# Kernel optimization log

Hardware: AMD Instinct MI355X
Metric: run time of the kernel (lower is better)

## Reference

```python
import jax, jax.numpy as jnp
import numpy as np


def _next_pow2(n: int) -> int:
    # matches torch: 2 ** ceil(log2(n))
    return 1 << (int(n) - 1).bit_length()


def setup_inputs() -> dict:
    key = jax.random.key(0)
    k1, k2 = jax.random.split(key)
    B, T, L = 256, 32768, 32768
    x = jax.random.normal(k1, (B, T), dtype=jnp.float32)
    filt = jax.random.normal(k2, (1, L), dtype=jnp.float32)
    return {"x": x, "filt": filt}


def reference(x, filt):
    """EpochedFutureFill.forward: exact causal convolution of x with filt.

    The per-token epoched algorithm (tau-step direct sum + FutureFill FFT
    cache refresh every K steps, cache initialized to zero) computes exactly
    y[b, t] = sum_{s=0}^{min(t, L-1)} filt[0, s] * x[b, t-s].
    We compute it with one FFT-based linear convolution, mirroring the
    float32 FFT math of future_fill().
    """
    B, T = x.shape
    L = filt.shape[-1]
    n_fft = _next_pow2(T + L - 1)
    xf = jnp.fft.rfft(x.astype(jnp.float32), n=n_fft)          # (B, n_fft//2+1)
    wf = jnp.fft.rfft(filt.astype(jnp.float32), n=n_fft)       # (1, n_fft//2+1)
    y = jnp.fft.irfft(xf * wf, n=n_fft)[:, :T]                 # causal lags 0..T-1
    return y.astype(x.dtype)
```

## Files before the change

### kernel.cpp

```cpp
#include <hip/hip_runtime.h>
#include <cstdint>

typedef __attribute__((ext_vector_type(8))) short short8;
typedef __attribute__((ext_vector_type(4))) float floatx4;

#define TWO_PI 6.283185307179586f

__device__ __forceinline__ unsigned short f2bf(float f) {
  union { float f; uint32_t u; } c; c.f = f;
  uint32_t u = c.u;
  u += 0x7FFFu + ((u >> 16) & 1u);
  return (unsigned short)(u >> 16);
}
__device__ __forceinline__ uint32_t packbf(float re, float im) {
  return (uint32_t)f2bf(re) | ((uint32_t)f2bf(im) << 16);
}


__global__ __launch_bounds__(256) void prep_all(
    const float* __restrict__ x, const float* __restrict__ filt,
    unsigned short* __restrict__ A1, unsigned short* __restrict__ A2,
    unsigned short* __restrict__ A3, unsigned short* __restrict__ A4,
    uint32_t* __restrict__ Zp, float2* __restrict__ Gw,
    float2* __restrict__ Tw) {
  const int bid = blockIdx.x;
  const int tid = threadIdx.x;
  const float w256 = TWO_PI / 256.0f;
  if (bid < 3072) {
    int idx = bid * 256 + tid;
    if (idx < 131072) {
      int col = idx & 255, row = idx >> 8;
      int k1 = row >> 1, d = row & 1, r = col >> 1, e = col & 1;
      float th = (float)((k1 * r) & 255) * w256;
      float sn, cs; __sincosf(th, &sn, &cs);
      A1[idx] = f2bf(d == 0 ? (e == 0 ? cs : sn) : (e == 0 ? -sn : cs));
    } else if (idx < 393216) {
      int j = idx - 131072;
      int col = j & 511, row = j >> 9;
      int k2 = row >> 1, d = row & 1, cc = col >> 1, e = col & 1;
      float th = (float)((k2 * cc) & 255) * w256;
      float sn, cs; __sincosf(th, &sn, &cs);
      A2[j] = f2bf(d == 0 ? (e == 0 ? cs : sn) : (e == 0 ? -sn : cs));
    } else if (idx < 655360) {
      int j = idx - 393216;
      int col = j & 511, row = j >> 9;
      int cc = row >> 1, d = row & 1, k2 = col >> 1, e = col & 1;
      float th = (float)((k2 * cc) & 255) * w256;
      float sn, cs; __sincosf(th, &sn, &cs);
      A3[j] = f2bf(d == 0 ? (e == 0 ? cs : -sn) : (e == 0 ? sn : cs));
    } else {
      int j = idx - 655360;
      int col = j & 511, row = j >> 9;
      int r = row >> 1, d = row & 1, k1 = col >> 1, e = col & 1;
      float th = (float)((k1 * r) & 255) * w256;
      float sn, cs; __sincosf(th, &sn, &cs);
      A4[j] = f2bf(d == 0 ? (e == 0 ? cs : -sn) : (e == 0 ? sn : cs));
    }
  } else if (bid < 4096) {
    int b2 = bid - 3072;
    int s = b2 >> 3, rq = b2 & 7;
    const float* x0 = x + (size_t)(2 * s) * 32768;
    const float* x1 = x0 + 32768;
    uint32_t v[16];
    #pragma unroll
    for (int rr = 0; rr < 16; ++rr) {
      int t = tid + 256 * (rq * 16 + rr);
      v[rr] = (uint32_t)f2bf(x0[t]) | ((uint32_t)f2bf(x1[t]) << 16);
    }
    uint32_t* dst = Zp + (size_t)(s * 256 + tid) * 128 + rq * 16;
    #pragma unroll
    for (int j = 0; j < 16; j += 4)
      *(uint4*)(dst + j) = make_uint4(v[j], v[j + 1], v[j + 2], v[j + 3]);
  } else if (bid < 4352) {
    int k1 = bid - 4096, c = tid;
    float ar = 0.f, ai = 0.f;
    for (int r = 0; r < 128; ++r) {
      float v = filt[c + 256 * r];
      float th = (float)((k1 * r) & 255) * w256;
      float sn, cs; __sincosf(th, &sn, &cs);
      ar += v * cs; ai -= v * sn;
    }
    float th = (float)((k1 * c) & 65535) * (TWO_PI / 65536.0f);
    float sn, cs; __sincosf(th, &sn, &cs);
    Gw[(k1 << 8) + c] = make_float2(ar * cs + ai * sn, ai * cs - ar * sn);
  } else {
    int k1 = bid - 4352, c = tid;
    float th = (float)((k1 * c) & 65535) * (TWO_PI / 65536.0f);
    float sn, cs; __sincosf(th, &sn, &cs);
    Tw[(k1 << 8) + c] = make_float2(cs, sn);
  }
}

__global__ __launch_bounds__(256) void prep_wb(const float2* __restrict__ Gw,
                                               float2* __restrict__ WtT) {
  int k1 = blockIdx.x, k2 = threadIdx.x;
  float ar = 0.f, ai = 0.f;
  for (int c = 0; c < 256; ++c) {
    float2 g = Gw[(k1 << 8) + c];
    float th = (float)((k2 * c) & 255) * (TWO_PI / 256.0f);
    float sn, cs; __sincosf(th, &sn, &cs);
    ar += g.x * cs + g.y * sn;
    ai += g.y * cs - g.x * sn;
  }
  WtT[(k2 << 8) + k1] = make_float2(ar, ai);
}

template <int MODE, int NCHUNK>
__global__ __launch_bounds__(256, 4) void dft_stage(
    const unsigned short* __restrict__ Af,
    const unsigned short* __restrict__ Bd,
    uint32_t* __restrict__ outp,
    float* __restrict__ yout,
    const float2* __restrict__ tab) {
  __shared__ unsigned short Sm[16384];
  constexpr int KP = NCHUNK * 32;

  const int mt = blockIdx.x >> 8;
  const int nt = blockIdx.x & 255;
  const int m0 = mt * 128, n0 = nt * 128;

  const int tid = threadIdx.x;
  const int w = tid >> 6, lane = tid & 63;
  const int qlo = lane & 15, qhi = lane >> 4;
  const int wr = w >> 1, wc = w & 1;
  const int rsub = lane >> 2;
  const int koff = ((lane & 3) ^ ((lane >> 3) & 3)) << 3;

  floatx4 acc[4][4];
  #pragma unroll
  for (int i = 0; i < 4; ++i)
    #pragma unroll
    for (int j = 0; j < 4; ++j) acc[i][j] = (floatx4){0.f, 0.f, 0.f, 0.f};

  auto issue = [&](int t) {
    const int buf = t & 1;
    const int k0 = t * 32;
    unsigned short* Asb = Sm + buf * 4096;
    unsigned short* Bsb = Sm + 8192 + buf * 4096;
    #pragma unroll
    for (int q = 0; q < 2; ++q) {
      const int rowbase = w * 32 + q * 16;
      const int R = rowbase + rsub;
      const unsigned short* gA = Af + (size_t)(m0 + R) * KP + k0 + koff;
      const unsigned short* gB = Bd + (size_t)(n0 + R) * KP + k0 + koff;
      __builtin_amdgcn_global_load_lds(
          (const __attribute__((address_space(1))) uint32_t*)gA,
          (__attribute__((address_space(3))) uint32_t*)&Asb[rowbase * 32], 16, 0, 0);
      __builtin_amdgcn_global_load_lds(
          (const __attribute__((address_space(1))) uint32_t*)gB,
          (__attribute__((address_space(3))) uint32_t*)&Bsb[rowbase * 32], 16, 0, 0);
    }
  };

  issue(0);
  #pragma unroll
  for (int t = 0; t < NCHUNK; ++t) {
    asm volatile("s_waitcnt vmcnt(0)" ::: "memory");
    __builtin_amdgcn_s_barrier();
    if (t + 1 < NCHUNK) issue(t + 1);
    __builtin_amdgcn_sched_barrier(0);
    const unsigned short* Ab = Sm + (t & 1) * 4096;
    const unsigned short* Bb = Sm + 8192 + (t & 1) * 4096;
    short8 a[4], bb[4];
    #pragma unroll
    for (int im = 0; im < 4; ++im) {
      const int R = wr * 64 + im * 16 + qlo;
      const int slot = qhi ^ ((R >> 1) & 3);
      a[im] = *(const short8*)&Ab[R * 32 + slot * 8];
    }
    #pragma unroll
    for (int in = 0; in < 4; ++in) {
      const int R = wc * 64 + in * 16 + qlo;
      const int slot = qhi ^ ((R >> 1) & 3);
      bb[in] = *(const short8*)&Bb[R * 32 + slot * 8];
    }
    __builtin_amdgcn_s_setprio(1);
    #pragma unroll
    for (int im = 0; im < 4; ++im)
      #pragma unroll
      for (int in = 0; in < 4; ++in)
        acc[im][in] = __builtin_amdgcn_mfma_f32_16x16x32_bf16(a[im], bb[in], acc[im][in], 0, 0, 0);
    __builtin_amdgcn_s_setprio(0);
  }

  const int s_idx = n0 >> 8;
  const int cl0 = n0 & 255;

  if (MODE == 2) {
    uint32_t* Tr = (uint32_t*)Sm;
    #pragma unroll
    for (int h = 0; h < 2; ++h) {
      __syncthreads();
      if (wc == h) {
        #pragma unroll
        for (int im = 0; im < 4; ++im) {
          const int mloc = wr * 32 + im * 8 + qhi * 2;
          #pragma unroll
          for (int in = 0; in < 4; ++in) {
            const int nl = in * 16 + qlo;
            #pragma unroll
            for (int pp = 0; pp < 2; ++pp) {
              const int mC = (m0 >> 1) + mloc + pp;
              float re = acc[im][in][2 * pp], iv = acc[im][in][2 * pp + 1];
              float2 wv = tab[(mC << 8) + cl0 + h * 64 + nl];
              float r2 = re * wv.x - iv * wv.y, i2 = re * wv.y + iv * wv.x;
              Tr[nl * 68 + mloc + pp] = packbf(r2, i2);
            }
          }
        }
      }
      __syncthreads();
      const int row = tid >> 2, qq = tid & 3;
      uint32_t* dst = outp + (size_t)((s_idx << 8) + cl0 + h * 64 + row) * 256 +
                      (m0 >> 1) + qq * 16;
      const uint32_t* srcp = Tr + row * 68 + qq * 16;
      #pragma unroll
      for (int j = 0; j < 16; j += 4)
        *(uint4*)(dst + j) = *(const uint4*)(srcp + j);
    }
    return;
  }

  #pragma unroll
  for (int im = 0; im < 4; ++im) {
    const int mloc = wr * 32 + im * 8 + qhi * 2;
    #pragma unroll
    for (int in = 0; in < 4; ++in) {
      const int nloc = wc * 64 + in * 16 + qlo;
      const int cloc = cl0 + nloc;
      #pragma unroll
      for (int pp = 0; pp < 2; ++pp) {
        const int mC = (m0 >> 1) + mloc + pp;
        float re = acc[im][in][2 * pp], iv = acc[im][in][2 * pp + 1];
        if (MODE == 1) {
          float2 tw = tab[(mC << 8) + cloc];
          float r2 = re * tw.x + iv * tw.y, i2 = iv * tw.x - re * tw.y;
          outp[(size_t)((s_idx << 8) + mC) * 256 + cloc] = packbf(r2, i2);
        } else if (MODE == 3) {
          float2 tw = tab[(mC << 8) + cloc];
          float r2 = re * tw.x - iv * tw.y, i2 = iv * tw.x + re * tw.y;
          outp[(size_t)((s_idx << 8) + mC) * 256 + cloc] = packbf(r2, i2);
        } else {
          const float sc = 1.0f / 65536.0f;
          float* y0 = yout + ((size_t)s_idx << 16) + (mC << 8) + cloc;
          y0[0] = re * sc;
          y0[32768] = iv * sc;
        }
      }
    }
  }
}

extern "C" void kernel_launch(void* const* d_in, const int* in_sizes, int n_in,
                              void* d_out, int out_size, void* d_ws, size_t ws_size,
                              hipStream_t stream) {
  const float* x = (const float*)d_in[0];
  const float* filt = (const float*)d_in[1];
  float* Y = (float*)d_out;

  char* ws = (char*)d_ws;
  unsigned short* A1 = (unsigned short*)(ws + 0);
  unsigned short* A2 = (unsigned short*)(ws + 0x40000);
  unsigned short* A3 = (unsigned short*)(ws + 0xC0000);
  unsigned short* A4 = (unsigned short*)(ws + 0x140000);
  float2* Gw  = (float2*)(ws + 0x180000);
  float2* WtT = (float2*)(ws + 0x200000);
  float2* Tw  = (float2*)(ws + 0x280000);
  unsigned short* Zp = (unsigned short*)(ws + (3u << 20));
  unsigned short* G2 = (unsigned short*)(ws + 19922944u);
  unsigned short* P  = (unsigned short*)(ws + 53477376u);
  unsigned short* H2 = (unsigned short*)(ws + (3u << 20));

  hipLaunchKernelGGL(prep_all, dim3(4608), dim3(256), 0, stream,
                     x, filt, A1, A2, A3, A4, (uint32_t*)Zp, Gw, Tw);
  hipLaunchKernelGGL(prep_wb, dim3(256), dim3(256), 0, stream, Gw, WtT);

  hipLaunchKernelGGL((dft_stage<1, 8>), dim3(1024), dim3(256), 0, stream,
                     A1, Zp, (uint32_t*)G2, (float*)nullptr, Tw);
  hipLaunchKernelGGL((dft_stage<2, 16>), dim3(1024), dim3(256), 0, stream,
                     A2, G2, (uint32_t*)P, (float*)nullptr, WtT);
  hipLaunchKernelGGL((dft_stage<3, 16>), dim3(1024), dim3(256), 0, stream,
                     A3, P, (uint32_t*)H2, (float*)nullptr, Tw);
  hipLaunchKernelGGL((dft_stage<4, 16>), dim3(512), dim3(256), 0, stream,
                     A4, H2, (uint32_t*)nullptr, Y, Tw);
}
```

Baseline: 199.8 us.

## Triple-buffer DFT GEMM LDS pipeline and precompute twiddle roots in shared memory

The DFT GEMM stage moves from a double-buffered to a triple-buffered LDS pipeline. It prefetches two chunks ahead and waits on a partial vmcnt so that global loads overlap more MFMA work. LDS per block grows, so the occupancy hint drops from 4 to 3 blocks per CU. The MODE 2 transpose epilogue now writes the whole 128-column tile in one pass using the larger shared buffer, instead of two halves separated by barriers. The prep kernels read a 256-entry root table from shared memory instead of calling sincos inside their inner loops.

```diff
diff --git a/kernel.cpp b/kernel.cpp
--- a/kernel.cpp
+++ b/kernel.cpp
@@ -23,6 +23,7 @@
     unsigned short* __restrict__ A3, unsigned short* __restrict__ A4,
     uint32_t* __restrict__ Zp, float2* __restrict__ Gw,
     float2* __restrict__ Tw) {
+  __shared__ float2 roots[256];
   const int bid = blockIdx.x;
   const int tid = threadIdx.x;
   const float w256 = TWO_PI / 256.0f;
@@ -73,12 +74,14 @@
       *(uint4*)(dst + j) = make_uint4(v[j], v[j + 1], v[j + 2], v[j + 3]);
   } else if (bid < 4352) {
     int k1 = bid - 4096, c = tid;
+    { float sn, cs; __sincosf((float)tid * w256, &sn, &cs);
+      roots[tid] = make_float2(cs, sn); }
+    __syncthreads();
     float ar = 0.f, ai = 0.f;
     for (int r = 0; r < 128; ++r) {
       float v = filt[c + 256 * r];
-      float th = (float)((k1 * r) & 255) * w256;
-      float sn, cs; __sincosf(th, &sn, &cs);
-      ar += v * cs; ai -= v * sn;
+      float2 wv = roots[(k1 * r) & 255];
+      ar += v * wv.x; ai -= v * wv.y;
     }
     float th = (float)((k1 * c) & 65535) * (TWO_PI / 65536.0f);
     float sn, cs; __sincosf(th, &sn, &cs);
@@ -93,26 +96,29 @@
 
 __global__ __launch_bounds__(256) void prep_wb(const float2* __restrict__ Gw,
                                                float2* __restrict__ WtT) {
+  __shared__ float2 roots[256];
   int k1 = blockIdx.x, k2 = threadIdx.x;
+  { float sn, cs; __sincosf((float)k2 * (TWO_PI / 256.0f), &sn, &cs);
+    roots[k2] = make_float2(cs, sn); }
+  __syncthreads();
   float ar = 0.f, ai = 0.f;
   for (int c = 0; c < 256; ++c) {
     float2 g = Gw[(k1 << 8) + c];
-    float th = (float)((k2 * c) & 255) * (TWO_PI / 256.0f);
-    float sn, cs; __sincosf(th, &sn, &cs);
-    ar += g.x * cs + g.y * sn;
-    ai += g.y * cs - g.x * sn;
+    float2 wv = roots[(k2 * c) & 255];
+    ar += g.x * wv.x + g.y * wv.y;
+    ai += g.y * wv.x - g.x * wv.y;
   }
   WtT[(k2 << 8) + k1] = make_float2(ar, ai);
 }
 
 template <int MODE, int NCHUNK>
-__global__ __launch_bounds__(256, 4) void dft_stage(
+__global__ __launch_bounds__(256, 3) void dft_stage(
     const unsigned short* __restrict__ Af,
     const unsigned short* __restrict__ Bd,
     uint32_t* __restrict__ outp,
     float* __restrict__ yout,
     const float2* __restrict__ tab) {
-  __shared__ unsigned short Sm[16384];
+  __shared__ unsigned short Sm[24576];
   constexpr int KP = NCHUNK * 32;
 
   const int mt = blockIdx.x >> 8;
@@ -133,10 +139,10 @@
     for (int j = 0; j < 4; ++j) acc[i][j] = (floatx4){0.f, 0.f, 0.f, 0.f};
 
   auto issue = [&](int t) {
-    const int buf = t & 1;
+    const int buf = t % 3;
     const int k0 = t * 32;
     unsigned short* Asb = Sm + buf * 4096;
-    unsigned short* Bsb = Sm + 8192 + buf * 4096;
+    unsigned short* Bsb = Sm + 12288 + buf * 4096;
     #pragma unroll
     for (int q = 0; q < 2; ++q) {
       const int rowbase = w * 32 + q * 16;
@@ -152,15 +158,16 @@
     }
   };
 
-  issue(0);
+  issue(0); issue(1);
   #pragma unroll
   for (int t = 0; t < NCHUNK; ++t) {
-    asm volatile("s_waitcnt vmcnt(0)" ::: "memory");
+    if (t + 1 < NCHUNK) asm volatile("s_waitcnt vmcnt(4)" ::: "memory");
+    else                asm volatile("s_waitcnt vmcnt(0)" ::: "memory");
     __builtin_amdgcn_s_barrier();
-    if (t + 1 < NCHUNK) issue(t + 1);
+    if (t + 2 < NCHUNK) issue(t + 2);
     __builtin_amdgcn_sched_barrier(0);
-    const unsigned short* Ab = Sm + (t & 1) * 4096;
-    const unsigned short* Bb = Sm + 8192 + (t & 1) * 4096;
+    const unsigned short* Ab = Sm + (t % 3) * 4096;
+    const unsigned short* Bb = Sm + 12288 + (t % 3) * 4096;
     short8 a[4], bb[4];
     #pragma unroll
     for (int im = 0; im < 4; ++im) {
@@ -187,37 +194,31 @@
   const int cl0 = n0 & 255;
 
   if (MODE == 2) {
+    __syncthreads();
     uint32_t* Tr = (uint32_t*)Sm;
     #pragma unroll
-    for (int h = 0; h < 2; ++h) {
-      __syncthreads();
-      if (wc == h) {
+    for (int im = 0; im < 4; ++im) {
+      const int mloc = wr * 32 + im * 8 + qhi * 2;
+      #pragma unroll
+      for (int in = 0; in < 4; ++in) {
+        const int nloc = wc * 64 + in * 16 + qlo;
         #pragma unroll
-        for (int im = 0; im < 4; ++im) {
-          const int mloc = wr * 32 + im * 8 + qhi * 2;
-          #pragma unroll
-          for (int in = 0; in < 4; ++in) {
-            const int nl = in * 16 + qlo;
-            #pragma unroll
-            for (int pp = 0; pp < 2; ++pp) {
-              const int mC = (m0 >> 1) + mloc + pp;
-              float re = acc[im][in][2 * pp], iv = acc[im][in][2 * pp + 1];
-              float2 wv = tab[(mC << 8) + cl0 + h * 64 + nl];
-              float r2 = re * wv.x - iv * wv.y, i2 = re * wv.y + iv * wv.x;
-              Tr[nl * 68 + mloc + pp] = packbf(r2, i2);
-            }
-          }
+        for (int pp = 0; pp < 2; ++pp) {
+          const int mC = (m0 >> 1) + mloc + pp;
+          float re = acc[im][in][2 * pp], iv = acc[im][in][2 * pp + 1];
+          float2 wv = tab[(mC << 8) + cl0 + nloc];
+          float r2 = re * wv.x - iv * wv.y, i2 = re * wv.y + iv * wv.x;
+          Tr[nloc * 68 + mloc + pp] = packbf(r2, i2);
         }
       }
-      __syncthreads();
-      const int row = tid >> 2, qq = tid & 3;
-      uint32_t* dst = outp + (size_t)((s_idx << 8) + cl0 + h * 64 + row) * 256 +
-                      (m0 >> 1) + qq * 16;
-      const uint32_t* srcp = Tr + row * 68 + qq * 16;
-      #pragma unroll
-      for (int j = 0; j < 16; j += 4)
-        *(uint4*)(dst + j) = *(const uint4*)(srcp + j);
-    }
+    }
+    __syncthreads();
+    const int ln = tid >> 1, half = tid & 1;
+    uint32_t* dst = outp + (size_t)((s_idx << 8) + cl0 + ln) * 256 + (m0 >> 1) + half * 32;
+    const uint32_t* srcp = Tr + ln * 68 + half * 32;
+    #pragma unroll
+    for (int j = 0; j < 32; j += 4)
+      *(uint4*)(dst + j) = *(const uint4*)(srcp + j);
     return;
   }
 
```

New measurement: 195.1 us. 1.02x faster.
